# Performance work log

Hardware: AMD Instinct MI355X
Metric: run time of the kernel (lower is better)

## Reference

```python
import jax, jax.numpy as jnp
import numpy as np
from jax import lax

ROUTING_ITERS = 3
EPS = 1e-8


def _conv(x, w, b, stride=1):
    # x: [B,C,H,W], w: [O,C,kh,kw]  (VALID padding, NCHW/OIHW)
    y = lax.conv_general_dilated(x, w, (stride, stride), 'VALID',
                                 dimension_numbers=('NCHW', 'OIHW', 'NCHW'))
    return y + b[None, :, None, None]


def _maxpool2(x):
    return lax.reduce_window(x, -jnp.inf, lax.max, (1, 1, 2, 2), (1, 1, 2, 2), 'VALID')


def _squash(s, axis=-1):
    n2 = jnp.sum(s * s, axis=axis, keepdims=True)
    return s * (n2 / (1.0 + n2)) / jnp.sqrt(n2 + EPS)


def setup_inputs() -> dict:
    key = jax.random.key(0)
    ks = jax.random.split(key, 9)
    p = lambda k, shp: (jax.random.normal(k, shp, dtype=jnp.float32) * 0.05)
    return {
        'x':  jax.random.normal(ks[0], (64, 1, 92, 92), dtype=jnp.float32),
        'w1': p(ks[1], (128, 1, 9, 9)),   'b1': jnp.zeros((128,), jnp.float32),
        'w2': p(ks[2], (64, 128, 5, 5)),  'b2': jnp.zeros((64,), jnp.float32),
        'wc': p(ks[3], (128, 64, 8, 8)),  'bc': jnp.zeros((128,), jnp.float32),
        # routing transform: [num_primary=1024, num_sar=10, out_dim=16, in_dim=32]
        'Wr': p(ks[4], (1024, 10, 16, 32)),
    }


def reference(x, w1, b1, w2, b2, wc, bc, Wr):
    B = x.shape[0]
    # feature extractor (dropout is identity at inference)
    h = jax.nn.relu(_conv(x, w1, b1))          # [B,128,84,84]
    h = _maxpool2(h)                            # [B,128,42,42]
    h = _conv(h, w2, b2)                        # [B,64,38,38]
    # primary capsule conv
    h = _conv(h, wc, bc, stride=2)              # [B,128,16,16]
    # 128 channels = 4 capsule types * 32-dim capsules, 16x16 spatial -> 1024 caps
    u = h.reshape(B, 4, 32, 16, 16).transpose(0, 1, 3, 4, 2).reshape(B, 1024, 32)
    u = _squash(u)                              # [B,1024,32]
    # u_hat: predictions of each primary cap for each SAR cap
    u_hat = jnp.einsum('bpi,ptoi->bpto', u, Wr)  # [B,1024,10,16]
    # dynamic routing
    b_log = jnp.zeros((B, 1024, 10), dtype=x.dtype)
    for _ in range(ROUTING_ITERS):
        c = jax.nn.softmax(b_log, axis=2)               # [B,1024,10]
        s = jnp.einsum('bpt,bpto->bto', c, u_hat)       # [B,10,16]
        v = _squash(s)                                   # [B,10,16]
        b_log = b_log + jnp.einsum('bpto,bto->bpt', u_hat, v)
    likelihood = jnp.sqrt(jnp.sum(v * v, axis=-1) + EPS)  # [B,10]
    return likelihood
```

## Files before the change

### kernel.cpp

```cpp
#include <hip/hip_runtime.h>
#include <hip/hip_bf16.h>
#include <math.h>


#define EPSF 1e-8f

typedef __bf16 bf16x8 __attribute__((ext_vector_type(8)));
typedef __bf16 bf16x4 __attribute__((ext_vector_type(4)));
typedef float floatx4 __attribute__((ext_vector_type(4)));
typedef float floatx16 __attribute__((ext_vector_type(16)));

__global__ __launch_bounds__(256) void k_t_w1b(const float* __restrict__ w1, __bf16* __restrict__ w1b) {
    int i = blockIdx.x * 256 + threadIdx.x;
    if (i >= 12288) return;
    int kt = i >> 10, oc = (i >> 3) & 127, j = i & 7;
    int k = kt * 8 + j;
    w1b[i] = (__bf16)(k < 81 ? w1[oc * 81 + k] : 0.f);
}

__global__ __launch_bounds__(256) void k_t_w2a(const float* __restrict__ w2, __bf16* __restrict__ w2a) {
    int i = blockIdx.x * 256 + threadIdx.x;
    if (i >= 204800) return;
    int j = i & 7, lane = (i >> 3) & 63, f = i >> 9;
    int mt = f & 1, ks = (f >> 1) & 3, rem = f >> 3;
    int khw = rem % 25, icc = rem / 25;
    int c32 = lane & 31, h = lane >> 5;
    int oc = mt * 32 + c32;
    int ic = icc * 64 + ks * 16 + h * 8 + j;
    w2a[i] = (__bf16)w2[(oc * 128 + ic) * 25 + khw];
}

__global__ __launch_bounds__(256) void k_t_wca(const float* __restrict__ wc, __bf16* __restrict__ wca) {
    int i = blockIdx.x * 256 + threadIdx.x;
    if (i >= 524288) return;
    int j = i & 7, lane = (i >> 3) & 63, f = i >> 9;
    int ct = f & 3, ks = (f >> 2) & 1, khw = (f >> 3) & 63, icc = f >> 9;
    int c32 = lane & 31, h = lane >> 5;
    int oc = ct * 32 + c32;
    int ic = icc * 32 + ks * 16 + h * 8 + j;
    wca[i] = (__bf16)wc[(oc * 64 + ic) * 64 + khw];
}

__global__ __launch_bounds__(256) void k_t_wrb(const float* __restrict__ Wr, __bf16* __restrict__ wrb) {
    int i = blockIdx.x * 256 + threadIdx.x;
    if (i >= 5242880) return;
    wrb[i] = (__bf16)Wr[i];
}

__global__ __launch_bounds__(256, 3) void k_conv1_mfma(const float* __restrict__ x,
                                                       const __bf16* __restrict__ w1b,
                                                       const float* __restrict__ b1,
                                                       __bf16* __restrict__ h1n) {
    __shared__ float xs[960];
    __shared__ __bf16 Bl[18432];
    int py = blockIdx.x, ocg = blockIdx.y, b = blockIdx.z;
    int t = threadIdx.x;
    int lane = t & 63, w = t >> 6;
    int cc = lane & 15, q = lane >> 4;

    const float* xb = x + (size_t)b * 8464 + 2 * py * 92;
    for (int j = t; j < 920; j += 256) xs[j] = xb[j];

    int ocA = ocg * 64 + w * 16 + cc;
    bf16x8 af[3];
#pragma unroll
    for (int ks = 0; ks < 3; ++ks)
        af[ks] = *(const bf16x8*)(w1b + ((ks * 4 + q) * 128 + ocA) * 8);

    __syncthreads();

    if (t < 192) {
        int row = t / 96, pos = t - (t / 96) * 96;
        int sbase = row * 92 + pos;
        bool pvalid = pos < 84;
#pragma unroll
        for (int kt = 0; kt < 12; ++kt) {
            bf16x8 pk;
#pragma unroll
            for (int j = 0; j < 8; ++j) {
                int k = kt * 8 + j;
                int kh = k / 9, kw = k - kh * 9;
                float v = (pvalid && k < 81) ? xs[sbase + kh * 92 + kw] : 0.f;
                pk[j] = (__bf16)v;
            }
            *(bf16x8*)(Bl + ((kt * 2 + row) * 96 + pos) * 8) = pk;
        }
    }
    __syncthreads();

    floatx4 acc[2][6];
    const char* Bb = (const char*)Bl + cc * 16 + q * 3072;
#pragma unroll
    for (int rr = 0; rr < 2; ++rr)
#pragma unroll
        for (int n6 = 0; n6 < 6; ++n6) {
            floatx4 a = (floatx4){0.f, 0.f, 0.f, 0.f};
#pragma unroll
            for (int ks = 0; ks < 3; ++ks) {
                bf16x8 bf = *(const bf16x8*)(Bb + ks * 12288 + rr * 1536 + n6 * 256);
                a = __builtin_amdgcn_mfma_f32_16x16x32_bf16(af[ks], bf, a, 0, 0, 0);
            }
            acc[rr][n6] = a;
        }

    int oc0 = ocg * 64 + w * 16 + q * 4;
    float4 bv = *(const float4*)(b1 + oc0);
    size_t obase = (((size_t)b * 42 + py) * 42) * 128 + oc0;
#pragma unroll
    for (int n6 = 0; n6 < 6; ++n6) {
        bf16x4 pk;
#pragma unroll
        for (int r = 0; r < 4; ++r) {
            float vert = fmaxf(acc[0][n6][r], acc[1][n6][r]);
            float hz = fmaxf(vert, __shfl_xor(vert, 1, 64));
            float pooled = fmaxf(hz + ((const float*)&bv)[r], 0.f);
            pk[r] = (__bf16)pooled;
        }
        if ((cc & 1) == 0) {
            int px = n6 * 8 + (cc >> 1);
            if (px < 42)
                *(bf16x4*)(h1n + obase + (size_t)px * 128) = pk;
        }
    }
}

__global__ __launch_bounds__(192, 2) void k_conv2(const __bf16* __restrict__ h1n,
                                                  const __bf16* __restrict__ w2a,
                                                  const float* __restrict__ b2,
                                                  __bf16* __restrict__ h2n) {
    __shared__ __bf16 ins[25704];
    int g = blockIdx.x, b = blockIdx.y;
    int row0 = g * 5;
    int t = threadIdx.x;
    int lane = t & 63, w = t >> 6;
    int c32 = lane & 31, h = lane >> 5;
    int validp = (g < 7) ? 190 : 114;

    int baseN[2], posi[2];
#pragma unroll
    for (int nt = 0; nt < 2; ++nt) {
        int pi = (w * 2 + nt) * 32 + c32;
        int pc = pi < validp ? pi : validp - 1;
        int r = pc / 38, c = pc - r * 38;
        posi[nt] = pi;
        baseN[nt] = (r * 42 + c) * 136 + h * 16;
    }
    floatx16 acc[2][2];
#pragma unroll
    for (int mt = 0; mt < 2; ++mt)
#pragma unroll
        for (int nt = 0; nt < 2; ++nt)
#pragma unroll
            for (int i = 0; i < 16; ++i) acc[mt][nt][i] = 0.f;

    for (int icc = 0; icc < 2; ++icc) {
        int ic0 = icc * 64;
        __syncthreads();
#pragma unroll
        for (int half = 0; half < 2; ++half) {
            uint4 rb[8];
            int lo[8];
#pragma unroll
            for (int k = 0; k < 8; ++k) {
                int j = (half * 8 + k) * 192 + t;
                if (j > 3023) j -= 192;
                int lr = j / 336, rem = j - lr * 336;
                int ix = rem >> 3, sb = rem & 7;
                int rg = row0 + lr; if (rg > 41) rg = 41;
                rb[k] = *(const uint4*)(h1n + ((((size_t)b * 42 + rg) * 42 + ix) * 128 + ic0 + sb * 8));
                lo[k] = (lr * 42 + ix) * 136 + sb * 16;
            }
#pragma unroll
            for (int k = 0; k < 8; ++k)
                *(uint4*)((char*)ins + lo[k]) = rb[k];
        }
        __syncthreads();
        const __bf16* wic = w2a + (size_t)icc * 25 * 4096 + (lane << 3);
#pragma unroll
        for (int khw = 0; khw < 25; ++khw) {
            int kh = khw / 5, kw = khw - kh * 5;
            int doff = (kh * 42 + kw) * 136;
            const __bf16* wk = wic + khw * 4096;
#pragma unroll
            for (int ks = 0; ks < 4; ++ks) {
                bf16x8 a0 = *(const bf16x8*)(wk + ks * 1024);
                bf16x8 a1 = *(const bf16x8*)(wk + ks * 1024 + 512);
#pragma unroll
                for (int nt = 0; nt < 2; ++nt) {
                    bf16x8 bfr = *(const bf16x8*)((char*)ins + baseN[nt] + doff + ks * 32);
                    acc[0][nt] = __builtin_amdgcn_mfma_f32_32x32x16_bf16(a0, bfr, acc[0][nt], 0, 0, 0);
                    acc[1][nt] = __builtin_amdgcn_mfma_f32_32x32x16_bf16(a1, bfr, acc[1][nt], 0, 0, 0);
                }
            }
        }
    }
#pragma unroll
    for (int nt = 0; nt < 2; ++nt) {
        int pi = posi[nt];
        if (pi < validp) {
            int r = pi / 38, c = pi - r * 38;
            int oh = row0 + r;
            size_t obase = (((size_t)b * 38 + oh) * 38 + c) * 64;
#pragma unroll
            for (int mt = 0; mt < 2; ++mt) {
#pragma unroll
                for (int g2 = 0; g2 < 4; ++g2) {
                    int oc0 = mt * 32 + g2 * 8 + h * 4;
                    float4 bv = *(const float4*)(b2 + oc0);
                    bf16x4 pk;
                    pk.x = (__bf16)(acc[mt][nt][g2 * 4 + 0] + bv.x);
                    pk.y = (__bf16)(acc[mt][nt][g2 * 4 + 1] + bv.y);
                    pk.z = (__bf16)(acc[mt][nt][g2 * 4 + 2] + bv.z);
                    pk.w = (__bf16)(acc[mt][nt][g2 * 4 + 3] + bv.w);
                    *(bf16x4*)(h2n + obase + oc0) = pk;
                }
            }
        }
    }
}

__global__ __launch_bounds__(256, 4) void k_convcaps(const __bf16* __restrict__ h2n,
                                                     const __bf16* __restrict__ wca,
                                                     const float* __restrict__ bc,
                                                     __bf16* __restrict__ ub) {
    __shared__ __bf16 ins[13680];
    int g = blockIdx.x, b = blockIdx.y;
    int t = threadIdx.x;
    int lane = t & 63, ct = t >> 6;
    int c32 = lane & 31, h = lane >> 5;
    int rloc = c32 >> 4, cx = c32 & 15;

    floatx16 acc;
#pragma unroll
    for (int i = 0; i < 16; ++i) acc[i] = 0.f;

    int Bbase = (76 * rloc + cx) * 72 + h * 16;
    for (int icc = 0; icc < 2; ++icc) {
        int ic0 = icc * 32;
        __syncthreads();
        {
            uint4 rb[6];
            int lo[6];
#pragma unroll
            for (int k = 0; k < 6; ++k) {
                int j = k * 256 + t;
                if (j > 1519) j -= 256;
                int r = j / 152, rem = j - r * 152;
                int c = rem >> 2, s = rem & 3;
                rb[k] = *(const uint4*)(h2n + ((((size_t)b * 38 + 4 * g + r) * 38 + c) * 64 + ic0 + s * 8));
                int X = (r * 2 + (c & 1)) * 19 + (c >> 1);
                lo[k] = X * 72 + s * 16;
            }
#pragma unroll
            for (int k = 0; k < 6; ++k)
                *(uint4*)((char*)ins + lo[k]) = rb[k];
        }
        __syncthreads();
        const __bf16* wic = wca + ((size_t)icc * 64 * 8 + ct) * 512 + (lane << 3);
#pragma unroll
        for (int khw = 0; khw < 64; ++khw) {
            int kh = khw >> 3, kw = khw & 7;
            int par = kw & 1, k2 = kw >> 1;
            int doff = ((kh * 2 + par) * 19 + k2) * 72;
            const __bf16* wk = wic + khw * 4096;
#pragma unroll
            for (int ks = 0; ks < 2; ++ks) {
                bf16x8 af = *(const bf16x8*)(wk + ks * 2048);
                bf16x8 bfr = *(const bf16x8*)((char*)ins + Bbase + doff + ks * 32);
                acc = __builtin_amdgcn_mfma_f32_32x32x16_bf16(af, bfr, acc, 0, 0, 0);
            }
        }
    }
    float vals[16];
    float n2p = 0.f;
#pragma unroll
    for (int g2 = 0; g2 < 4; ++g2) {
        float4 bv = *(const float4*)(bc + ct * 32 + g2 * 8 + h * 4);
#pragma unroll
        for (int j = 0; j < 4; ++j) {
            float v = acc[g2 * 4 + j] + ((const float*)&bv)[j];
            vals[g2 * 4 + j] = v;
            n2p = fmaf(v, v, n2p);
        }
    }
    float n2 = n2p + __shfl_xor(n2p, 32, 64);
    float scale = (n2 / (1.f + n2)) / sqrtf(n2 + EPSF);
    int pos = (2 * g + rloc) * 16 + cx;
    __bf16* dst = ub + (((size_t)b * 1024 + ct * 256 + pos) * 32);
#pragma unroll
    for (int g2 = 0; g2 < 4; ++g2) {
        bf16x4 pk;
        pk.x = (__bf16)(vals[g2 * 4 + 0] * scale);
        pk.y = (__bf16)(vals[g2 * 4 + 1] * scale);
        pk.z = (__bf16)(vals[g2 * 4 + 2] * scale);
        pk.w = (__bf16)(vals[g2 * 4 + 3] * scale);
        *(bf16x4*)(dst + g2 * 8 + h * 4) = pk;
    }
}

__global__ __launch_bounds__(256, 2) void k_uhat(const __bf16* __restrict__ ub,
                                                 const __bf16* __restrict__ wrb,
                                                 __bf16* __restrict__ uhT) {
    int pt = blockIdx.x, ts = blockIdx.y, bz = blockIdx.z;
    int t = threadIdx.x;
    int p = pt * 64 + (t & 63);
    int q = t >> 6;
    bf16x8 wf[4][4];
#pragma unroll
    for (int o4 = 0; o4 < 4; ++o4)
#pragma unroll
        for (int j = 0; j < 4; ++j)
            wf[o4][j] = *(const bf16x8*)(wrb + (((size_t)p * 10 + ts) * 16 + q * 4 + o4) * 32 + j * 8);
#pragma unroll 1
    for (int bi = 0; bi < 16; ++bi) {
        int b = bz * 16 + bi;
        bf16x8 uf[4];
        const bf16x8* up = (const bf16x8*)(ub + ((size_t)b * 1024 + p) * 32);
#pragma unroll
        for (int j = 0; j < 4; ++j) uf[j] = up[j];
#pragma unroll
        for (int o4 = 0; o4 < 4; ++o4) {
            float s = 0.f;
#pragma unroll
            for (int j = 0; j < 4; ++j)
#pragma unroll
                for (int e = 0; e < 8; ++e)
                    s = fmaf((float)uf[j][e], (float)wf[o4][j][e], s);
            uhT[(((size_t)b * 10 + ts) * 16 + q * 4 + o4) * 1024 + p] = (__bf16)s;
        }
    }
}

__global__ __launch_bounds__(256) void k_route_s(const __bf16* __restrict__ uhT,
                                                 const float* __restrict__ bl,
                                                 float* __restrict__ vout,
                                                 float* __restrict__ out,
                                                 int first, int last) {
    __shared__ float sred[4][16];
    int b = blockIdx.x, tt = blockIdx.y;
    int t = threadIdx.x;
    float acc[16];
#pragma unroll
    for (int o = 0; o < 16; ++o) acc[o] = 0.f;
    const float* blb = bl + b * 10240;
    const __bf16* uhb = uhT + ((size_t)b * 10 + tt) * 16384;
    for (int p = t; p < 1024; p += 256) {
        float c;
        if (first) {
            c = 0.1f;
        } else {
            float den = 0.f, et = 0.f;
#pragma unroll
            for (int tp = 0; tp < 10; ++tp) {
                float e = expf(blb[tp * 1024 + p]);
                den += e;
                if (tp == tt) et = e;
            }
            c = et / den;
        }
#pragma unroll
        for (int o = 0; o < 16; ++o)
            acc[o] = fmaf(c, (float)uhb[o * 1024 + p], acc[o]);
    }
    int lane = t & 63, wid = t >> 6;
#pragma unroll
    for (int o = 0; o < 16; ++o) {
        float v = acc[o];
#pragma unroll
        for (int off = 32; off >= 1; off >>= 1) v += __shfl_xor(v, off, 64);
        if (lane == 0) sred[wid][o] = v;
    }
    __syncthreads();
    if (t < 16) {
        float s = (sred[0][t] + sred[1][t]) + (sred[2][t] + sred[3][t]);
        float n2 = s * s;
#pragma unroll
        for (int off = 1; off < 16; off <<= 1) n2 += __shfl_xor(n2, off, 16);
        float scale = (n2 / (1.f + n2)) / sqrtf(n2 + EPSF);
        vout[(b * 10 + tt) * 16 + t] = s * scale;
        if (last && t == 0) {
            float sv2 = n2 * scale * scale;
            out[b * 10 + tt] = sqrtf(sv2 + EPSF);
        }
    }
}

__global__ __launch_bounds__(256) void k_route_b(const __bf16* __restrict__ uhT,
                                                 const float* __restrict__ vv,
                                                 float* __restrict__ bl,
                                                 int first) {
    __shared__ float vs[16];
    int b = blockIdx.x, tt = blockIdx.y;
    int t = threadIdx.x;
    if (t < 16) vs[t] = vv[(b * 10 + tt) * 16 + t];
    __syncthreads();
    const __bf16* uhb = uhT + ((size_t)b * 10 + tt) * 16384;
    float* blb = bl + (b * 10 + tt) * 1024;
    for (int p = t; p < 1024; p += 256) {
        float d = 0.f;
#pragma unroll
        for (int o = 0; o < 16; ++o) d = fmaf((float)uhb[o * 1024 + p], vs[o], d);
        blb[p] = first ? d : (blb[p] + d);
    }
}

extern "C" void kernel_launch(void* const* d_in, const int* in_sizes, int n_in,
                              void* d_out, int out_size, void* d_ws, size_t ws_size,
                              hipStream_t stream) {
    const float* x  = (const float*)d_in[0];
    const float* w1 = (const float*)d_in[1];
    const float* b1 = (const float*)d_in[2];
    const float* w2 = (const float*)d_in[3];
    const float* b2 = (const float*)d_in[4];
    const float* wc = (const float*)d_in[5];
    const float* bc = (const float*)d_in[6];
    const float* Wr = (const float*)d_in[7];
    float* out = (float*)d_out;
    float* ws  = (float*)d_ws;

    __bf16* w2a = (__bf16*)(ws);
    __bf16* wca = (__bf16*)(ws + 102400);
    __bf16* w1b = (__bf16*)(ws + 364544);
    __bf16* h1n = (__bf16*)(ws + 375040);
    __bf16* h2n = (__bf16*)(ws + 7600384);
    __bf16* ub  = (__bf16*)(ws + 12654848);
    float*  bl  = ws + 14752000;
    float*  vv  = ws + 15407360;
    __bf16* wrb = (__bf16*)(ws + 15417600);
    __bf16* uhT = (__bf16*)(ws + 375040);

    k_t_w1b<<<48, 256, 0, stream>>>(w1, w1b);
    k_t_w2a<<<800, 256, 0, stream>>>(w2, w2a);
    k_t_wca<<<2048, 256, 0, stream>>>(wc, wca);
    k_t_wrb<<<20480, 256, 0, stream>>>(Wr, wrb);
    k_conv1_mfma<<<dim3(42, 2, 64), 256, 0, stream>>>(x, w1b, b1, h1n);
    k_conv2<<<dim3(8, 64), 192, 0, stream>>>(h1n, w2a, b2, h2n);
    k_convcaps<<<dim3(8, 64), 256, 0, stream>>>(h2n, wca, bc, ub);
    k_uhat<<<dim3(16, 10, 4), 256, 0, stream>>>(ub, wrb, uhT);
    k_route_s<<<dim3(64, 10), 256, 0, stream>>>(uhT, bl, vv, out, 1, 0);
    k_route_b<<<dim3(64, 10), 256, 0, stream>>>(uhT, vv, bl, 1);
    k_route_s<<<dim3(64, 10), 256, 0, stream>>>(uhT, bl, vv, out, 0, 0);
    k_route_b<<<dim3(64, 10), 256, 0, stream>>>(uhT, vv, bl, 0);
    k_route_s<<<dim3(64, 10), 256, 0, stream>>>(uhT, bl, vv, out, 0, 1);
}
```

Before: 326.8 us.

## Split conv2 input-channel reduction across grid z and sum partials in convcaps

Conv2 now launches a third grid dimension over the two input-channel halves. Each block computes a partial sum and writes it to its own fp32 buffer. The convcaps staging loop then adds the two partials plus the bias and converts to bf16 before storing to shared memory. This doubles conv2's block count (512 to 1024) to improve occupancy and load balance across CUs. In exchange it writes and reads two fp32 partial tensors instead of one bf16 tensor, roughly four times the intermediate traffic.

```diff
diff --git a/kernel.cpp b/kernel.cpp
--- a/kernel.cpp
+++ b/kernel.cpp
@@ -126,15 +126,15 @@
 
 __global__ __launch_bounds__(192, 2) void k_conv2(const __bf16* __restrict__ h1n,
                                                   const __bf16* __restrict__ w2a,
-                                                  const float* __restrict__ b2,
-                                                  __bf16* __restrict__ h2n) {
+                                                  float* __restrict__ p01) {
     __shared__ __bf16 ins[25704];
-    int g = blockIdx.x, b = blockIdx.y;
+    int g = blockIdx.x, b = blockIdx.y, icc = blockIdx.z;
     int row0 = g * 5;
     int t = threadIdx.x;
     int lane = t & 63, w = t >> 6;
     int c32 = lane & 31, h = lane >> 5;
     int validp = (g < 7) ? 190 : 114;
+    int ic0 = icc * 64;
 
     int baseN[2], posi[2];
 #pragma unroll
@@ -145,6 +145,26 @@
         posi[nt] = pi;
         baseN[nt] = (r * 42 + c) * 136 + h * 16;
     }
+
+#pragma unroll
+    for (int half = 0; half < 2; ++half) {
+        uint4 rb[8];
+        int lo[8];
+#pragma unroll
+        for (int k = 0; k < 8; ++k) {
+            int j = (half * 8 + k) * 192 + t;
+            if (j > 3023) j -= 192;
+            int lr = j / 336, rem = j - lr * 336;
+            int ix = rem >> 3, sb = rem & 7;
+            int rg = row0 + lr; if (rg > 41) rg = 41;
+            rb[k] = *(const uint4*)(h1n + ((((size_t)b * 42 + rg) * 42 + ix) * 128 + ic0 + sb * 8));
+            lo[k] = (lr * 42 + ix) * 136 + sb * 16;
+        }
+#pragma unroll
+        for (int k = 0; k < 8; ++k)
+            *(uint4*)((char*)ins + lo[k]) = rb[k];
+    }
+
     floatx16 acc[2][2];
 #pragma unroll
     for (int mt = 0; mt < 2; ++mt)
@@ -153,47 +173,26 @@
 #pragma unroll
             for (int i = 0; i < 16; ++i) acc[mt][nt][i] = 0.f;
 
-    for (int icc = 0; icc < 2; ++icc) {
-        int ic0 = icc * 64;
-        __syncthreads();
-#pragma unroll
-        for (int half = 0; half < 2; ++half) {
-            uint4 rb[8];
-            int lo[8];
-#pragma unroll
-            for (int k = 0; k < 8; ++k) {
-                int j = (half * 8 + k) * 192 + t;
-                if (j > 3023) j -= 192;
-                int lr = j / 336, rem = j - lr * 336;
-                int ix = rem >> 3, sb = rem & 7;
-                int rg = row0 + lr; if (rg > 41) rg = 41;
-                rb[k] = *(const uint4*)(h1n + ((((size_t)b * 42 + rg) * 42 + ix) * 128 + ic0 + sb * 8));
-                lo[k] = (lr * 42 + ix) * 136 + sb * 16;
-            }
-#pragma unroll
-            for (int k = 0; k < 8; ++k)
-                *(uint4*)((char*)ins + lo[k]) = rb[k];
-        }
-        __syncthreads();
-        const __bf16* wic = w2a + (size_t)icc * 25 * 4096 + (lane << 3);
-#pragma unroll
-        for (int khw = 0; khw < 25; ++khw) {
-            int kh = khw / 5, kw = khw - kh * 5;
-            int doff = (kh * 42 + kw) * 136;
-            const __bf16* wk = wic + khw * 4096;
-#pragma unroll
-            for (int ks = 0; ks < 4; ++ks) {
-                bf16x8 a0 = *(const bf16x8*)(wk + ks * 1024);
-                bf16x8 a1 = *(const bf16x8*)(wk + ks * 1024 + 512);
-#pragma unroll
-                for (int nt = 0; nt < 2; ++nt) {
-                    bf16x8 bfr = *(const bf16x8*)((char*)ins + baseN[nt] + doff + ks * 32);
-                    acc[0][nt] = __builtin_amdgcn_mfma_f32_32x32x16_bf16(a0, bfr, acc[0][nt], 0, 0, 0);
-                    acc[1][nt] = __builtin_amdgcn_mfma_f32_32x32x16_bf16(a1, bfr, acc[1][nt], 0, 0, 0);
-                }
-            }
-        }
-    }
+    __syncthreads();
+    const __bf16* wic = w2a + (size_t)icc * 25 * 4096 + (lane << 3);
+#pragma unroll
+    for (int khw = 0; khw < 25; ++khw) {
+        int kh = khw / 5, kw = khw - kh * 5;
+        int doff = (kh * 42 + kw) * 136;
+        const __bf16* wk = wic + khw * 4096;
+#pragma unroll
+        for (int ks = 0; ks < 4; ++ks) {
+            bf16x8 a0 = *(const bf16x8*)(wk + ks * 1024);
+            bf16x8 a1 = *(const bf16x8*)(wk + ks * 1024 + 512);
+#pragma unroll
+            for (int nt = 0; nt < 2; ++nt) {
+                bf16x8 bfr = *(const bf16x8*)((char*)ins + baseN[nt] + doff + ks * 32);
+                acc[0][nt] = __builtin_amdgcn_mfma_f32_32x32x16_bf16(a0, bfr, acc[0][nt], 0, 0, 0);
+                acc[1][nt] = __builtin_amdgcn_mfma_f32_32x32x16_bf16(a1, bfr, acc[1][nt], 0, 0, 0);
+            }
+        }
+    }
+    float* pdst = p01 + (size_t)icc * 5914624;
 #pragma unroll
     for (int nt = 0; nt < 2; ++nt) {
         int pi = posi[nt];
@@ -206,21 +205,21 @@
 #pragma unroll
                 for (int g2 = 0; g2 < 4; ++g2) {
                     int oc0 = mt * 32 + g2 * 8 + h * 4;
-                    float4 bv = *(const float4*)(b2 + oc0);
-                    bf16x4 pk;
-                    pk.x = (__bf16)(acc[mt][nt][g2 * 4 + 0] + bv.x);
-                    pk.y = (__bf16)(acc[mt][nt][g2 * 4 + 1] + bv.y);
-                    pk.z = (__bf16)(acc[mt][nt][g2 * 4 + 2] + bv.z);
-                    pk.w = (__bf16)(acc[mt][nt][g2 * 4 + 3] + bv.w);
-                    *(bf16x4*)(h2n + obase + oc0) = pk;
+                    floatx4 pv;
+                    pv[0] = acc[mt][nt][g2 * 4 + 0];
+                    pv[1] = acc[mt][nt][g2 * 4 + 1];
+                    pv[2] = acc[mt][nt][g2 * 4 + 2];
+                    pv[3] = acc[mt][nt][g2 * 4 + 3];
+                    *(floatx4*)(pdst + obase + oc0) = pv;
                 }
             }
         }
     }
 }
 
-__global__ __launch_bounds__(256, 4) void k_convcaps(const __bf16* __restrict__ h2n,
+__global__ __launch_bounds__(256, 4) void k_convcaps(const float* __restrict__ p01,
                                                      const __bf16* __restrict__ wca,
+                                                     const float* __restrict__ b2,
                                                      const float* __restrict__ bc,
                                                      __bf16* __restrict__ ub) {
     __shared__ __bf16 ins[13680];
@@ -238,22 +237,36 @@
     for (int icc = 0; icc < 2; ++icc) {
         int ic0 = icc * 32;
         __syncthreads();
-        {
-            uint4 rb[6];
-            int lo[6];
-#pragma unroll
-            for (int k = 0; k < 6; ++k) {
-                int j = k * 256 + t;
+#pragma unroll
+        for (int bt = 0; bt < 3; ++bt) {
+            floatx4 rA[2], rB[2], rC[2], rD[2], bL[2], bH[2];
+            int lo[2];
+#pragma unroll
+            for (int k = 0; k < 2; ++k) {
+                int j = (bt * 2 + k) * 256 + t;
                 if (j > 1519) j -= 256;
                 int r = j / 152, rem = j - r * 152;
                 int c = rem >> 2, s = rem & 3;
-                rb[k] = *(const uint4*)(h2n + ((((size_t)b * 38 + 4 * g + r) * 38 + c) * 64 + ic0 + s * 8));
+                size_t bf = ((((size_t)b * 38 + 4 * g + r) * 38 + c) * 64 + ic0 + s * 8);
+                rA[k] = *(const floatx4*)(p01 + bf);
+                rB[k] = *(const floatx4*)(p01 + bf + 4);
+                rC[k] = *(const floatx4*)(p01 + 5914624 + bf);
+                rD[k] = *(const floatx4*)(p01 + 5914624 + bf + 4);
+                bL[k] = *(const floatx4*)(b2 + ic0 + s * 8);
+                bH[k] = *(const floatx4*)(b2 + ic0 + s * 8 + 4);
                 int X = (r * 2 + (c & 1)) * 19 + (c >> 1);
                 lo[k] = X * 72 + s * 16;
             }
 #pragma unroll
-            for (int k = 0; k < 6; ++k)
-                *(uint4*)((char*)ins + lo[k]) = rb[k];
+            for (int k = 0; k < 2; ++k) {
+                bf16x8 pk;
+#pragma unroll
+                for (int e = 0; e < 4; ++e) {
+                    pk[e]     = (__bf16)(rA[k][e] + rC[k][e] + bL[k][e]);
+                    pk[4 + e] = (__bf16)(rB[k][e] + rD[k][e] + bH[k][e]);
+                }
+                *(bf16x8*)((char*)ins + lo[k]) = pk;
+            }
         }
         __syncthreads();
         const __bf16* wic = wca + ((size_t)icc * 64 * 8 + ct) * 512 + (lane << 3);
@@ -422,11 +435,11 @@
     __bf16* wca = (__bf16*)(ws + 102400);
     __bf16* w1b = (__bf16*)(ws + 364544);
     __bf16* h1n = (__bf16*)(ws + 375040);
-    __bf16* h2n = (__bf16*)(ws + 7600384);
     __bf16* ub  = (__bf16*)(ws + 12654848);
     float*  bl  = ws + 14752000;
     float*  vv  = ws + 15407360;
     __bf16* wrb = (__bf16*)(ws + 15417600);
+    float*  p01 = ws + 18039040;
     __bf16* uhT = (__bf16*)(ws + 375040);
 
     k_t_w1b<<<48, 256, 0, stream>>>(w1, w1b);
@@ -434,8 +447,8 @@
     k_t_wca<<<2048, 256, 0, stream>>>(wc, wca);
     k_t_wrb<<<20480, 256, 0, stream>>>(Wr, wrb);
     k_conv1_mfma<<<dim3(42, 2, 64), 256, 0, stream>>>(x, w1b, b1, h1n);
-    k_conv2<<<dim3(8, 64), 192, 0, stream>>>(h1n, w2a, b2, h2n);
-    k_convcaps<<<dim3(8, 64), 256, 0, stream>>>(h2n, wca, bc, ub);
+    k_conv2<<<dim3(8, 64, 2), 192, 0, stream>>>(h1n, w2a, p01);
+    k_convcaps<<<dim3(8, 64), 256, 0, stream>>>(p01, wca, b2, bc, ub);
     k_uhat<<<dim3(16, 10, 4), 256, 0, stream>>>(ub, wrb, uhT);
     k_route_s<<<dim3(64, 10), 256, 0, stream>>>(uhT, bl, vv, out, 1, 0);
     k_route_b<<<dim3(64, 10), 256, 0, stream>>>(uhT, vv, bl, 1);
```

Result: slower. 344.1 us (+5.3%).

## Split conv2 over input-channel halves with fp32 partials and a reduce kernel

Applied to the files above, without the earlier changes.

Conv2 now launches a third grid dimension over the two 64-channel input chunks, so each block loads one chunk and does half the MFMA work. Each block writes fp32 partial sums to a workspace buffer. A new reduction kernel adds the two partials and the bias, then writes the bf16 activation. This is meant to raise parallelism and occupancy for conv2, at the cost of extra global memory traffic for the fp32 partials and an additional kernel launch.

```diff
diff --git a/kernel.cpp b/kernel.cpp
--- a/kernel.cpp
+++ b/kernel.cpp
@@ -126,15 +126,15 @@
 
 __global__ __launch_bounds__(192, 2) void k_conv2(const __bf16* __restrict__ h1n,
                                                   const __bf16* __restrict__ w2a,
-                                                  const float* __restrict__ b2,
-                                                  __bf16* __restrict__ h2n) {
+                                                  float* __restrict__ p01) {
     __shared__ __bf16 ins[25704];
-    int g = blockIdx.x, b = blockIdx.y;
+    int g = blockIdx.x, b = blockIdx.y, icc = blockIdx.z;
     int row0 = g * 5;
     int t = threadIdx.x;
     int lane = t & 63, w = t >> 6;
     int c32 = lane & 31, h = lane >> 5;
     int validp = (g < 7) ? 190 : 114;
+    int ic0 = icc * 64;
 
     int baseN[2], posi[2];
 #pragma unroll
@@ -145,6 +145,26 @@
         posi[nt] = pi;
         baseN[nt] = (r * 42 + c) * 136 + h * 16;
     }
+
+#pragma unroll
+    for (int half = 0; half < 2; ++half) {
+        uint4 rb[8];
+        int lo[8];
+#pragma unroll
+        for (int k = 0; k < 8; ++k) {
+            int j = (half * 8 + k) * 192 + t;
+            if (j > 3023) j -= 192;
+            int lr = j / 336, rem = j - lr * 336;
+            int ix = rem >> 3, sb = rem & 7;
+            int rg = row0 + lr; if (rg > 41) rg = 41;
+            rb[k] = *(const uint4*)(h1n + ((((size_t)b * 42 + rg) * 42 + ix) * 128 + ic0 + sb * 8));
+            lo[k] = (lr * 42 + ix) * 136 + sb * 16;
+        }
+#pragma unroll
+        for (int k = 0; k < 8; ++k)
+            *(uint4*)((char*)ins + lo[k]) = rb[k];
+    }
+
     floatx16 acc[2][2];
 #pragma unroll
     for (int mt = 0; mt < 2; ++mt)
@@ -153,47 +173,26 @@
 #pragma unroll
             for (int i = 0; i < 16; ++i) acc[mt][nt][i] = 0.f;
 
-    for (int icc = 0; icc < 2; ++icc) {
-        int ic0 = icc * 64;
-        __syncthreads();
-#pragma unroll
-        for (int half = 0; half < 2; ++half) {
-            uint4 rb[8];
-            int lo[8];
-#pragma unroll
-            for (int k = 0; k < 8; ++k) {
-                int j = (half * 8 + k) * 192 + t;
-                if (j > 3023) j -= 192;
-                int lr = j / 336, rem = j - lr * 336;
-                int ix = rem >> 3, sb = rem & 7;
-                int rg = row0 + lr; if (rg > 41) rg = 41;
-                rb[k] = *(const uint4*)(h1n + ((((size_t)b * 42 + rg) * 42 + ix) * 128 + ic0 + sb * 8));
-                lo[k] = (lr * 42 + ix) * 136 + sb * 16;
-            }
-#pragma unroll
-            for (int k = 0; k < 8; ++k)
-                *(uint4*)((char*)ins + lo[k]) = rb[k];
-        }
-        __syncthreads();
-        const __bf16* wic = w2a + (size_t)icc * 25 * 4096 + (lane << 3);
-#pragma unroll
-        for (int khw = 0; khw < 25; ++khw) {
-            int kh = khw / 5, kw = khw - kh * 5;
-            int doff = (kh * 42 + kw) * 136;
-            const __bf16* wk = wic + khw * 4096;
-#pragma unroll
-            for (int ks = 0; ks < 4; ++ks) {
-                bf16x8 a0 = *(const bf16x8*)(wk + ks * 1024);
-                bf16x8 a1 = *(const bf16x8*)(wk + ks * 1024 + 512);
-#pragma unroll
-                for (int nt = 0; nt < 2; ++nt) {
-                    bf16x8 bfr = *(const bf16x8*)((char*)ins + baseN[nt] + doff + ks * 32);
-                    acc[0][nt] = __builtin_amdgcn_mfma_f32_32x32x16_bf16(a0, bfr, acc[0][nt], 0, 0, 0);
-                    acc[1][nt] = __builtin_amdgcn_mfma_f32_32x32x16_bf16(a1, bfr, acc[1][nt], 0, 0, 0);
-                }
-            }
-        }
-    }
+    __syncthreads();
+    const __bf16* wic = w2a + (size_t)icc * 25 * 4096 + (lane << 3);
+#pragma unroll
+    for (int khw = 0; khw < 25; ++khw) {
+        int kh = khw / 5, kw = khw - kh * 5;
+        int doff = (kh * 42 + kw) * 136;
+        const __bf16* wk = wic + khw * 4096;
+#pragma unroll
+        for (int ks = 0; ks < 4; ++ks) {
+            bf16x8 a0 = *(const bf16x8*)(wk + ks * 1024);
+            bf16x8 a1 = *(const bf16x8*)(wk + ks * 1024 + 512);
+#pragma unroll
+            for (int nt = 0; nt < 2; ++nt) {
+                bf16x8 bfr = *(const bf16x8*)((char*)ins + baseN[nt] + doff + ks * 32);
+                acc[0][nt] = __builtin_amdgcn_mfma_f32_32x32x16_bf16(a0, bfr, acc[0][nt], 0, 0, 0);
+                acc[1][nt] = __builtin_amdgcn_mfma_f32_32x32x16_bf16(a1, bfr, acc[1][nt], 0, 0, 0);
+            }
+        }
+    }
+    float* pdst = p01 + (size_t)icc * 5914624;
 #pragma unroll
     for (int nt = 0; nt < 2; ++nt) {
         int pi = posi[nt];
@@ -206,17 +205,33 @@
 #pragma unroll
                 for (int g2 = 0; g2 < 4; ++g2) {
                     int oc0 = mt * 32 + g2 * 8 + h * 4;
-                    float4 bv = *(const float4*)(b2 + oc0);
-                    bf16x4 pk;
-                    pk.x = (__bf16)(acc[mt][nt][g2 * 4 + 0] + bv.x);
-                    pk.y = (__bf16)(acc[mt][nt][g2 * 4 + 1] + bv.y);
-                    pk.z = (__bf16)(acc[mt][nt][g2 * 4 + 2] + bv.z);
-                    pk.w = (__bf16)(acc[mt][nt][g2 * 4 + 3] + bv.w);
-                    *(bf16x4*)(h2n + obase + oc0) = pk;
+                    floatx4 pv;
+                    pv[0] = acc[mt][nt][g2 * 4 + 0];
+                    pv[1] = acc[mt][nt][g2 * 4 + 1];
+                    pv[2] = acc[mt][nt][g2 * 4 + 2];
+                    pv[3] = acc[mt][nt][g2 * 4 + 3];
+                    *(floatx4*)(pdst + obase + oc0) = pv;
                 }
             }
         }
     }
+}
+
+__global__ __launch_bounds__(256) void k_reduce_h2(const float* __restrict__ p01,
+                                                   const float* __restrict__ b2,
+                                                   __bf16* __restrict__ h2n) {
+    int i = blockIdx.x * 256 + threadIdx.x;
+    if (i >= 1478656) return;
+    size_t e = (size_t)i * 4;
+    floatx4 a = *(const floatx4*)(p01 + e);
+    floatx4 b = *(const floatx4*)(p01 + 5914624 + e);
+    floatx4 bv = *(const floatx4*)(b2 + ((i * 4) & 63));
+    bf16x4 pk;
+    pk.x = (__bf16)(a[0] + b[0] + bv[0]);
+    pk.y = (__bf16)(a[1] + b[1] + bv[1]);
+    pk.z = (__bf16)(a[2] + b[2] + bv[2]);
+    pk.w = (__bf16)(a[3] + b[3] + bv[3]);
+    *(bf16x4*)(h2n + e) = pk;
 }
 
 __global__ __launch_bounds__(256, 4) void k_convcaps(const __bf16* __restrict__ h2n,
@@ -427,6 +442,7 @@
     float*  bl  = ws + 14752000;
     float*  vv  = ws + 15407360;
     __bf16* wrb = (__bf16*)(ws + 15417600);
+    float*  p01 = ws + 18039040;
     __bf16* uhT = (__bf16*)(ws + 375040);
 
     k_t_w1b<<<48, 256, 0, stream>>>(w1, w1b);
@@ -434,7 +450,8 @@
     k_t_wca<<<2048, 256, 0, stream>>>(wc, wca);
     k_t_wrb<<<20480, 256, 0, stream>>>(Wr, wrb);
     k_conv1_mfma<<<dim3(42, 2, 64), 256, 0, stream>>>(x, w1b, b1, h1n);
-    k_conv2<<<dim3(8, 64), 192, 0, stream>>>(h1n, w2a, b2, h2n);
+    k_conv2<<<dim3(8, 64, 2), 192, 0, stream>>>(h1n, w2a, p01);
+    k_reduce_h2<<<5776, 256, 0, stream>>>(p01, b2, h2n);
     k_convcaps<<<dim3(8, 64), 256, 0, stream>>>(h2n, wca, bc, ub);
     k_uhat<<<dim3(16, 10, 4), 256, 0, stream>>>(ub, wrb, uhT);
     k_route_s<<<dim3(64, 10), 256, 0, stream>>>(uhT, bl, vv, out, 1, 0);
```

After: 324.0 us. No clear change (-0.9%).
